# Optimization experiments

Hardware: AMD Instinct MI355X
Metric: run time of the kernel (lower is better)

The kernel has to match this reference:

```python
import jax, jax.numpy as jnp
import numpy as np

B, K, U, D = 4096, 32, 16384, 256


def setup_inputs() -> dict:
    key = jax.random.key(0)
    k1, k2, k3 = jax.random.split(key, 3)
    neigh_idx = jax.random.randint(k1, (B, K), 0, U, dtype=jnp.int32)
    # emulate samp_neigh.union({node_id}): guarantee self index in each row
    neigh_idx = neigh_idx.at[:, 0].set(jnp.arange(B, dtype=jnp.int32))
    features_table = jax.random.normal(k2, (U, D), dtype=jnp.float32)
    noise_table = jax.random.normal(k3, (U, D), dtype=jnp.float32)
    return {"neigh_idx": neigh_idx, "features_table": features_table, "noise_table": noise_table}


def reference(neigh_idx, features_table, noise_table):
    # Dense binary mask [B, U]; duplicates collapse via .set (set semantics, as in torch mask[r,c]=1.0)
    rows = jnp.arange(neigh_idx.shape[0])[:, None]
    mask = jnp.zeros((neigh_idx.shape[0], features_table.shape[0]), features_table.dtype)
    mask = mask.at[rows, neigh_idx].set(1.0)
    # symmetric GCN normalization: mask / sqrt(rowsum) / sqrt(colsum)
    row_n = jnp.sqrt(mask.sum(axis=1, keepdims=True))  # >= 1 (self-loop present)
    col_n = jnp.sqrt(mask.sum(axis=0, keepdims=True))
    # In torch, unique_nodes_list only contains referenced nodes, so no zero columns.
    # Guard zero columns (mask entries there are 0, so result is unchanged vs torch).
    col_n = jnp.where(col_n > 0, col_n, 1.0)
    m = mask / row_n / col_n  # [B, U]
    to_feats = m @ features_table       # [B, D]
    to_noise_feats = m @ noise_table    # [B, D]
    return (to_feats, to_noise_feats)
```

## Files before the change

### kernel.cpp

```cpp
#include <hip/hip_runtime.h>


#define B_ 4096
#define K_ 32
#define U_ 16384
#define D_ 256
#define HALF_SLOTS (U_ * D_ / 8)

typedef unsigned int uint4n __attribute__((ext_vector_type(4)));

__device__ __forceinline__ unsigned bf16_rne(float x) {
    const unsigned u = __float_as_uint(x);
    return (u + 0x7FFFu + ((u >> 16) & 1u)) >> 16;
}
__device__ __forceinline__ unsigned pack2(float lo, float hi) {
    return bf16_rne(lo) | (bf16_rne(hi) << 16);
}
__device__ __forceinline__ float blo(unsigned v) { return __uint_as_float(v << 16); }
__device__ __forceinline__ float bhi(unsigned v) { return __uint_as_float(v & 0xFFFF0000u); }

__device__ __forceinline__ void conv_slot(const float4* __restrict__ src,
                                          uint4n* __restrict__ packed,
                                          int t, int half_off) {
    const int u = t >> 5;
    const int s = t & 31;
    const float4 a = src[u * (D_ / 4) + s * 2];
    const float4 b = src[u * (D_ / 4) + s * 2 + 1];
    uint4n o;
    o.x = pack2(a.x, a.y);
    o.y = pack2(a.z, a.w);
    o.z = pack2(b.x, b.y);
    o.w = pack2(b.z, b.w);
    __builtin_nontemporal_store(o, &packed[u * 64 + half_off + s]);
}

__global__ __launch_bounds__(256) void gcn_prep_feat(const float4* __restrict__ feat,
                                                     uint4n* __restrict__ packed,
                                                     int* __restrict__ colcnt) {
    const int gid = blockIdx.x * 256 + threadIdx.x;
    if (gid < U_) colcnt[gid] = 0;
    conv_slot(feat, packed, gid, 0);
}

__global__ __launch_bounds__(256) void gcn_prep_noise(const int* __restrict__ idx,
                                                      const float4* __restrict__ noise,
                                                      uint4n* __restrict__ packed,
                                                      int* __restrict__ colcnt) {
    const int gid = blockIdx.x * 256 + threadIdx.x;
    conv_slot(noise, packed, gid, 32);

    const int wg = gid >> 6;
    if (wg < B_) {
        const int lane = threadIdx.x & 63;
        const int kk = lane & 31;
        const int u = idx[wg * K_ + kk];
        bool dup = false;
        #pragma unroll
        for (int j = 0; j < K_; ++j) {
            const int uj = __shfl(u, j);
            if (j < kk && uj == u) dup = true;
        }
        if (lane < 32 && !dup) atomicAdd(&colcnt[u], 1);
    }
}

__global__ __launch_bounds__(256) void gcn_gather(const int* __restrict__ idx,
                                                  const uint4n* __restrict__ packed,
                                                  const int* __restrict__ colcnt,
                                                  float4* __restrict__ out) {
    const int row = blockIdx.x * 4 + (threadIdx.x >> 6);
    const int lane = threadIdx.x & 63;

    const int kk = lane & 31;
    const int u = idx[row * K_ + kk];

    bool dup = false;
    #pragma unroll
    for (int j = 0; j < K_; ++j) {
        const int uj = __shfl(u, j);
        if (j < kk && uj == u) dup = true;
    }
    const int rowcnt = __popcll(__ballot(!dup) & 0xFFFFFFFFull);

    float w = 0.0f;
    if (!dup) w = rsqrtf((float)(rowcnt * colcnt[u]));

    int us[K_]; float wk[K_];
    #pragma unroll
    for (int k = 0; k < K_; ++k) {
        us[k] = __builtin_amdgcn_readlane(u, k);
        wk[k] = __uint_as_float(
            (unsigned)__builtin_amdgcn_readlane((int)__float_as_uint(w), k));
    }

    float a0 = 0.f, a1 = 0.f, a2 = 0.f, a3 = 0.f;
    float a4 = 0.f, a5 = 0.f, a6 = 0.f, a7 = 0.f;

    #pragma unroll
    for (int k = 0; k < K_; ++k) {
        const uint4n v = packed[us[k] * 64 + lane];
        const float wkk = wk[k];
        a0 = fmaf(wkk, blo(v.x), a0);
        a1 = fmaf(wkk, bhi(v.x), a1);
        a2 = fmaf(wkk, blo(v.y), a2);
        a3 = fmaf(wkk, bhi(v.y), a3);
        a4 = fmaf(wkk, blo(v.z), a4);
        a5 = fmaf(wkk, bhi(v.z), a5);
        a6 = fmaf(wkk, blo(v.w), a6);
        a7 = fmaf(wkk, bhi(v.w), a7);
    }

    const int base = (lane < 32)
        ? (row * (D_ / 4) + lane * 2)
        : (B_ * (D_ / 4) + row * (D_ / 4) + (lane - 32) * 2);
    out[base]     = make_float4(a0, a1, a2, a3);
    out[base + 1] = make_float4(a4, a5, a6, a7);
}

extern "C" void kernel_launch(void* const* d_in, const int* in_sizes, int n_in,
                              void* d_out, int out_size, void* d_ws, size_t ws_size,
                              hipStream_t stream) {
    const int*    idx   = (const int*)d_in[0];
    const float4* feat  = (const float4*)d_in[1];
    const float4* noise = (const float4*)d_in[2];
    float4*       out   = (float4*)d_out;

    uint4n* packed = (uint4n*)d_ws;
    int*    colcnt = (int*)((char*)d_ws + 32u * 1024 * 1024);

    gcn_prep_feat <<<HALF_SLOTS / 256, 256, 0, stream>>>(feat, packed, colcnt);
    gcn_prep_noise<<<HALF_SLOTS / 256, 256, 0, stream>>>(idx, noise, packed, colcnt);
    gcn_gather    <<<B_ / 4,          256, 0, stream>>>(idx, packed, colcnt, out);
}
```

Before: 40.20 us.

## Fold column normalization into bf16 table prep and skip duplicate gathers

Column counts are now computed in separate zero and count kernels before the conversion pass. The conversion then pre-scales each packed bf16 row by rsqrt(colcnt), so the gather only sums raw rows and applies a single row factor at the end. Duplicate neighbours are skipped inside the gather loop instead of being loaded with zero weight. The packed stores are also no longer nontemporal, so they may stay in cache for the gather. In exchange there is one more kernel launch and a serial dependency from the count kernel to the conversion pass, and unreferenced rows get scaled by inf but are never read.

```diff
diff --git a/kernel.cpp b/kernel.cpp
--- a/kernel.cpp
+++ b/kernel.cpp
@@ -19,54 +19,49 @@
 __device__ __forceinline__ float blo(unsigned v) { return __uint_as_float(v << 16); }
 __device__ __forceinline__ float bhi(unsigned v) { return __uint_as_float(v & 0xFFFF0000u); }
 
-__device__ __forceinline__ void conv_slot(const float4* __restrict__ src,
-                                          uint4n* __restrict__ packed,
-                                          int t, int half_off) {
-    const int u = t >> 5;
-    const int s = t & 31;
+__global__ __launch_bounds__(256) void gcn_zero(int4* __restrict__ colcnt4) {
+    colcnt4[blockIdx.x * 256 + threadIdx.x] = make_int4(0, 0, 0, 0);
+}
+
+__global__ __launch_bounds__(256) void gcn_colcount(const int* __restrict__ idx,
+                                                    int* __restrict__ colcnt) {
+    const int row = blockIdx.x * 4 + (threadIdx.x >> 6);
+    const int lane = threadIdx.x & 63;
+    const int kk = lane & 31;
+    const int u = idx[row * K_ + kk];
+    bool dup = false;
+    #pragma unroll
+    for (int j = 0; j < K_; ++j) {
+        const int uj = __shfl(u, j);
+        if (j < kk && uj == u) dup = true;
+    }
+    if (lane < 32 && !dup) atomicAdd(&colcnt[u], 1);
+}
+
+__global__ __launch_bounds__(256) void gcn_prep(const float4* __restrict__ feat,
+                                                const float4* __restrict__ noise,
+                                                const int* __restrict__ colcnt,
+                                                uint4n* __restrict__ packed) {
+    const int t = blockIdx.x * 256 + threadIdx.x;
+    const bool isNoise = t >= HALF_SLOTS;
+    const int tt = isNoise ? t - HALF_SLOTS : t;
+    const int u = tt >> 5;
+    const int s = tt & 31;
+    const float4* src = isNoise ? noise : feat;
+
+    const float cf = rsqrtf((float)colcnt[u]);
     const float4 a = src[u * (D_ / 4) + s * 2];
     const float4 b = src[u * (D_ / 4) + s * 2 + 1];
     uint4n o;
-    o.x = pack2(a.x, a.y);
-    o.y = pack2(a.z, a.w);
-    o.z = pack2(b.x, b.y);
-    o.w = pack2(b.z, b.w);
-    __builtin_nontemporal_store(o, &packed[u * 64 + half_off + s]);
-}
-
-__global__ __launch_bounds__(256) void gcn_prep_feat(const float4* __restrict__ feat,
-                                                     uint4n* __restrict__ packed,
-                                                     int* __restrict__ colcnt) {
-    const int gid = blockIdx.x * 256 + threadIdx.x;
-    if (gid < U_) colcnt[gid] = 0;
-    conv_slot(feat, packed, gid, 0);
-}
-
-__global__ __launch_bounds__(256) void gcn_prep_noise(const int* __restrict__ idx,
-                                                      const float4* __restrict__ noise,
-                                                      uint4n* __restrict__ packed,
-                                                      int* __restrict__ colcnt) {
-    const int gid = blockIdx.x * 256 + threadIdx.x;
-    conv_slot(noise, packed, gid, 32);
-
-    const int wg = gid >> 6;
-    if (wg < B_) {
-        const int lane = threadIdx.x & 63;
-        const int kk = lane & 31;
-        const int u = idx[wg * K_ + kk];
-        bool dup = false;
-        #pragma unroll
-        for (int j = 0; j < K_; ++j) {
-            const int uj = __shfl(u, j);
-            if (j < kk && uj == u) dup = true;
-        }
-        if (lane < 32 && !dup) atomicAdd(&colcnt[u], 1);
-    }
+    o.x = pack2(a.x * cf, a.y * cf);
+    o.y = pack2(a.z * cf, a.w * cf);
+    o.z = pack2(b.x * cf, b.y * cf);
+    o.w = pack2(b.z * cf, b.w * cf);
+    packed[u * 64 + (isNoise ? 32 : 0) + s] = o;
 }
 
 __global__ __launch_bounds__(256) void gcn_gather(const int* __restrict__ idx,
                                                   const uint4n* __restrict__ packed,
-                                                  const int* __restrict__ colcnt,
                                                   float4* __restrict__ out) {
     const int row = blockIdx.x * 4 + (threadIdx.x >> 6);
     const int lane = threadIdx.x & 63;
@@ -80,41 +75,33 @@
         const int uj = __shfl(u, j);
         if (j < kk && uj == u) dup = true;
     }
-    const int rowcnt = __popcll(__ballot(!dup) & 0xFFFFFFFFull);
+    const unsigned uniq = (unsigned)(__ballot(!dup) & 0xFFFFFFFFull);
+    const float rowfac = rsqrtf((float)__popc(uniq));
 
-    float w = 0.0f;
-    if (!dup) w = rsqrtf((float)(rowcnt * colcnt[u]));
-
-    int us[K_]; float wk[K_];
+    int us[K_];
     #pragma unroll
-    for (int k = 0; k < K_; ++k) {
+    for (int k = 0; k < K_; ++k)
         us[k] = __builtin_amdgcn_readlane(u, k);
-        wk[k] = __uint_as_float(
-            (unsigned)__builtin_amdgcn_readlane((int)__float_as_uint(w), k));
-    }
 
     float a0 = 0.f, a1 = 0.f, a2 = 0.f, a3 = 0.f;
     float a4 = 0.f, a5 = 0.f, a6 = 0.f, a7 = 0.f;
 
     #pragma unroll
     for (int k = 0; k < K_; ++k) {
-        const uint4n v = packed[us[k] * 64 + lane];
-        const float wkk = wk[k];
-        a0 = fmaf(wkk, blo(v.x), a0);
-        a1 = fmaf(wkk, bhi(v.x), a1);
-        a2 = fmaf(wkk, blo(v.y), a2);
-        a3 = fmaf(wkk, bhi(v.y), a3);
-        a4 = fmaf(wkk, blo(v.z), a4);
-        a5 = fmaf(wkk, bhi(v.z), a5);
-        a6 = fmaf(wkk, blo(v.w), a6);
-        a7 = fmaf(wkk, bhi(v.w), a7);
+        if ((uniq >> k) & 1u) {
+            const uint4n v = packed[us[k] * 64 + lane];
+            a0 += blo(v.x); a1 += bhi(v.x);
+            a2 += blo(v.y); a3 += bhi(v.y);
+            a4 += blo(v.z); a5 += bhi(v.z);
+            a6 += blo(v.w); a7 += bhi(v.w);
+        }
     }
 
     const int base = (lane < 32)
         ? (row * (D_ / 4) + lane * 2)
         : (B_ * (D_ / 4) + row * (D_ / 4) + (lane - 32) * 2);
-    out[base]     = make_float4(a0, a1, a2, a3);
-    out[base + 1] = make_float4(a4, a5, a6, a7);
+    out[base]     = make_float4(a0 * rowfac, a1 * rowfac, a2 * rowfac, a3 * rowfac);
+    out[base + 1] = make_float4(a4 * rowfac, a5 * rowfac, a6 * rowfac, a7 * rowfac);
 }
 
 extern "C" void kernel_launch(void* const* d_in, const int* in_sizes, int n_in,
@@ -128,7 +115,8 @@
     uint4n* packed = (uint4n*)d_ws;
     int*    colcnt = (int*)((char*)d_ws + 32u * 1024 * 1024);
 
-    gcn_prep_feat <<<HALF_SLOTS / 256, 256, 0, stream>>>(feat, packed, colcnt);
-    gcn_prep_noise<<<HALF_SLOTS / 256, 256, 0, stream>>>(idx, noise, packed, colcnt);
-    gcn_gather    <<<B_ / 4,          256, 0, stream>>>(idx, packed, colcnt, out);
+    gcn_zero    <<<U_ / 1024,           256, 0, stream>>>((int4*)colcnt);
+    gcn_colcount<<<B_ / 4,              256, 0, stream>>>(idx, colcnt);
+    gcn_prep    <<<2 * HALF_SLOTS / 256, 256, 0, stream>>>(feat, noise, colcnt, packed);
+    gcn_gather  <<<B_ / 4,              256, 0, stream>>>(idx, packed, out);
 }
```

After: 44.99 us. 1.12x slower.
